# Optimization experiments

Hardware: AMD Instinct MI355X
Metric: run time of the kernel (lower is better)

The kernel has to match this reference:

```python
import jax, jax.numpy as jnp
import numpy as np

N = 50000      # nodes
E = 800000     # edges (avg degree 16)
H = 128        # hidden_nf
NORM_FACTOR = 100.0   # normalization_factor, aggregation 'sum'
NORM_CONST = 1.0      # norm_constant (effective_constant = max(1, 1.0))
EPS = 1e-8


def silu(v):
    return v * jax.nn.sigmoid(v)


def setup_inputs() -> dict:
    key = jax.random.key(0)
    ks = jax.random.split(key, 16)
    IN_E = 2 * H + 2  # edge MLP input: h[row] | h[col] | [radial, edge_attr]

    def w(k, shape, scale=0.05):
        return jax.random.normal(k, shape, dtype=jnp.float32) * scale

    return {
        "h": jax.random.normal(ks[0], (N, H), dtype=jnp.float32),
        "x": jax.random.normal(ks[1], (N, 3), dtype=jnp.float32),
        "edge_index": jax.random.randint(ks[2], (2, E), 0, N, dtype=jnp.int32),
        "edge_attr": jax.random.normal(ks[3], (E, 1), dtype=jnp.float32),
        "node_mask": jnp.ones((N, 1), dtype=jnp.float32),
        "edge_mask": jnp.ones((E, 1), dtype=jnp.float32),
        # 2 stacked GCL layers (identical shapes -> stacked on leading dim)
        "gcl_e_w1": w(ks[4], (2, IN_E, H)), "gcl_e_b1": jnp.zeros((2, H), jnp.float32),
        "gcl_e_w2": w(ks[5], (2, H, H)),    "gcl_e_b2": jnp.zeros((2, H), jnp.float32),
        "gcl_a_w":  w(ks[6], (2, H, 1)),    "gcl_a_b":  jnp.zeros((2, 1), jnp.float32),
        "gcl_n_w1": w(ks[7], (2, 2 * H, H)),"gcl_n_b1": jnp.zeros((2, H), jnp.float32),
        "gcl_n_w2": w(ks[8], (2, H, H)),    "gcl_n_b2": jnp.zeros((2, H), jnp.float32),
        # EquivariantUpdate coord MLP (last layer xavier gain 0.001 -> tiny, no bias)
        "c_w1": w(ks[9], (IN_E, H)), "c_b1": jnp.zeros((H,), jnp.float32),
        "c_w2": w(ks[10], (H, H)),   "c_b2": jnp.zeros((H,), jnp.float32),
        "c_w3": w(ks[11], (H, 1), 0.001),
    }


def reference(h, x, edge_index, edge_attr, node_mask, edge_mask,
              gcl_e_w1, gcl_e_b1, gcl_e_w2, gcl_e_b2, gcl_a_w, gcl_a_b,
              gcl_n_w1, gcl_n_b1, gcl_n_w2, gcl_n_b2,
              c_w1, c_b1, c_w2, c_b2, c_w3):
    row, col = edge_index[0], edge_index[1]
    n_nodes = h.shape[0]

    # coord2diff
    diff = x[row] - x[col]                                  # [E,3]
    radial = jnp.sum(diff * diff, axis=1, keepdims=True)    # [E,1]
    norm = jnp.sqrt(radial + EPS)
    coord_diff = diff / (norm + NORM_CONST)

    # edge_attr = cat([distances, edge_attr])  -> edge_feat_nf = 2
    ea = jnp.concatenate([radial, edge_attr], axis=1)       # [E,2]

    # n_layers=2 GCLs with attention
    for i in range(2):
        einp = jnp.concatenate([h[row], h[col], ea], axis=1)             # [E,258]
        mij = silu(silu(einp @ gcl_e_w1[i] + gcl_e_b1[i]) @ gcl_e_w2[i] + gcl_e_b2[i])
        att = jax.nn.sigmoid(mij @ gcl_a_w[i] + gcl_a_b[i])
        ef = mij * att * edge_mask                                       # [E,H]
        agg = jax.ops.segment_sum(ef, row, num_segments=n_nodes) / NORM_FACTOR
        ninp = jnp.concatenate([h, agg], axis=1)                         # [N,2H]
        h = h + (silu(ninp @ gcl_n_w1[i] + gcl_n_b1[i]) @ gcl_n_w2[i] + gcl_n_b2[i])
        h = h * node_mask

    # EquivariantUpdate (tanh=False, reflection_equiv=True -> no cross term)
    einp = jnp.concatenate([h[row], h[col], ea], axis=1)
    phi = silu(silu(einp @ c_w1 + c_b1) @ c_w2 + c_b2) @ c_w3            # [E,1]
    trans = coord_diff * phi * edge_mask                                 # [E,3]
    aggx = jax.ops.segment_sum(trans, row, num_segments=n_nodes) / NORM_FACTOR
    x = (x + aggx) * node_mask

    h = h * node_mask
    return (h, x)
```

## Files before the change

kernel.cpp:

```cpp
#include <hip/hip_runtime.h>
#include <hip/hip_bf16.h>
#include <math.h>
#include <string.h>

#define DEV __device__ __forceinline__

typedef __bf16 bf16;
typedef bf16 bf16x8 __attribute__((ext_vector_type(8)));
typedef bf16 bf16x2 __attribute__((ext_vector_type(2)));
typedef float f32x4 __attribute__((ext_vector_type(4)));
typedef unsigned int uint;

constexpr int N_NODES = 50000;
constexpr int N_EDGES = 800000;
constexpr int H = 128;
constexpr int NB_SCAN = (N_NODES + 255) / 256;

DEV float fsilu(float x) { return x / (1.f + __expf(-x)); }
DEV float fsigmoid(float x) { return 1.f / (1.f + __expf(-x)); }


__global__ void transpose_pad_kernel(bf16* __restrict__ dst, const float* __restrict__ src,
                                     int K, int Nf, int KP) {
    int idx = blockIdx.x * 256 + threadIdx.x;
    if (idx >= Nf * KP) return;
    int n = idx / KP, k = idx - n * KP;
    dst[idx] = (k < K) ? (bf16)src[k * Nf + n] : (bf16)0.f;
}

__global__ void h_init_kernel(const float* __restrict__ h, float* __restrict__ h_cur,
                              bf16* __restrict__ h_bf, int n) {
    int i = blockIdx.x * 256 + threadIdx.x;
    if (i < n) { float v = h[i]; h_cur[i] = v; h_bf[i] = (bf16)v; }
}

__global__ void ea_kernel(const float* __restrict__ x, const int* __restrict__ ei,
                          const float* __restrict__ eattr, bf16* __restrict__ ea_bf) {
    int e = blockIdx.x * 256 + threadIdx.x;
    if (e >= N_EDGES) return;
    int r = ei[e], c = ei[N_EDGES + e];
    float dx = x[r * 3 + 0] - x[c * 3 + 0];
    float dy = x[r * 3 + 1] - x[c * 3 + 1];
    float dz = x[r * 3 + 2] - x[c * 3 + 2];
    float radial = dx * dx + dy * dy + dz * dz;
    ea_bf[e * 2 + 0] = (bf16)radial;
    ea_bf[e * 2 + 1] = (bf16)eattr[e];
}

__global__ void out_h_kernel(const float* __restrict__ h_cur, const float* __restrict__ nmask,
                             float* __restrict__ out) {
    int i = blockIdx.x * 256 + threadIdx.x;
    if (i < N_NODES * H) out[i] = h_cur[i] * nmask[i >> 7];
}


__global__ void count_kernel(const int* __restrict__ ei, int* __restrict__ deg) {
    int e = blockIdx.x * 256 + threadIdx.x;
    if (e < N_EDGES) atomicAdd(&deg[ei[e]], 1);
}

__global__ void scan1_kernel(const int* __restrict__ deg, int* __restrict__ off,
                             int* __restrict__ bsum) {
    __shared__ int s[256];
    int t = threadIdx.x, i = blockIdx.x * 256 + t;
    int v = (i < N_NODES) ? deg[i] : 0;
    s[t] = v;
    __syncthreads();
#pragma unroll
    for (int st = 1; st < 256; st <<= 1) {
        int x = (t >= st) ? s[t - st] : 0;
        __syncthreads();
        s[t] += x;
        __syncthreads();
    }
    if (i < N_NODES) off[i] = s[t] - v;
    if (t == 255) bsum[blockIdx.x] = s[255];
}

__global__ void scan2_kernel(int* __restrict__ bsum) {
    __shared__ int s[256];
    int t = threadIdx.x;
    int v = (t < NB_SCAN) ? bsum[t] : 0;
    s[t] = v;
    __syncthreads();
#pragma unroll
    for (int st = 1; st < 256; st <<= 1) {
        int x = (t >= st) ? s[t - st] : 0;
        __syncthreads();
        s[t] += x;
        __syncthreads();
    }
    if (t < NB_SCAN) bsum[t] = s[t] - v;
}

__global__ void scan3_kernel(int* __restrict__ off, int* __restrict__ cursor,
                             const int* __restrict__ bsum) {
    int i = blockIdx.x * 256 + threadIdx.x;
    if (i >= N_NODES) return;
    int o = off[i] + bsum[blockIdx.x];
    off[i] = o;
    cursor[i] = o;
}

__global__ void fill_kernel(const int* __restrict__ ei, int* __restrict__ cursor,
                            int* __restrict__ eids) {
    int e = blockIdx.x * 256 + threadIdx.x;
    if (e >= N_EDGES) return;
    int slot = atomicAdd(&cursor[ei[e]], 1);
    eids[slot] = e;
}


__global__ __launch_bounds__(256) void gather_h_kernel(
    const bf16* __restrict__ ef, const int* __restrict__ off, const int* __restrict__ deg,
    const int* __restrict__ eids, bf16* __restrict__ agg_bf) {
    int t = threadIdx.x, lane = t & 63, wv = t >> 6;
    int n = blockIdx.x * 4 + wv;
    if (n >= N_NODES) return;
    int st = off[n], dg = deg[n];
    float s0 = 0.f, s1 = 0.f;
    for (int k = 0; k < dg; ++k) {
        int e = eids[st + k];
        uint v = *(const uint*)(ef + (size_t)e * H + lane * 2);
        s0 += __uint_as_float(v << 16);
        s1 += __uint_as_float(v & 0xffff0000u);
    }
    bf16x2 o;
    o[0] = (bf16)(s0 * 0.01f);
    o[1] = (bf16)(s1 * 0.01f);
    *(bf16x2*)(agg_bf + (size_t)n * H + lane * 2) = o;
}

__global__ __launch_bounds__(256) void gather_x_kernel(
    const float* __restrict__ trans, const int* __restrict__ off, const int* __restrict__ deg,
    const int* __restrict__ eids, const float* __restrict__ x, const float* __restrict__ nmask,
    float* __restrict__ outx) {
    int t = threadIdx.x, lane = t & 63, wv = t >> 6;
    int n = blockIdx.x * 4 + wv;
    if (n >= N_NODES) return;
    int st = off[n], dg = deg[n];
    float sx = 0.f, sy = 0.f, sz = 0.f;
    for (int k = lane; k < dg; k += 64) {
        int e = eids[st + k];
        sx += trans[e * 3 + 0];
        sy += trans[e * 3 + 1];
        sz += trans[e * 3 + 2];
    }
#pragma unroll
    for (int m = 1; m < 64; m <<= 1) {
        sx += __shfl_xor(sx, m);
        sy += __shfl_xor(sy, m);
        sz += __shfl_xor(sz, m);
    }
    if (lane == 0) {
        float nm = nmask[n];
        outx[n * 3 + 0] = (x[n * 3 + 0] + sx * 0.01f) * nm;
        outx[n * 3 + 1] = (x[n * 3 + 1] + sy * 0.01f) * nm;
        outx[n * 3 + 2] = (x[n * 3 + 2] + sz * 0.01f) * nm;
    }
}


template <int KCHUNKS, int ASTRIDE, int BSTRIDE>
DEV void wave_gemm(const bf16* A_lds, const bf16* __restrict__ Bt,
                   f32x4 (&acc)[4][2], int lr, int lg, int wv) {
#pragma unroll
    for (int kk = 0; kk < KCHUNKS; ++kk) {
        int ko = kk * 32 + lg * 8;
        bf16x8 a[4], b[2];
#pragma unroll
        for (int er = 0; er < 4; ++er)
            a[er] = *(const bf16x8*)(A_lds + (er * 16 + lr) * ASTRIDE + ko);
#pragma unroll
        for (int j = 0; j < 2; ++j)
            b[j] = *(const bf16x8*)(Bt + (size_t)((wv * 2 + j) * 16 + lr) * BSTRIDE + ko);
#pragma unroll
        for (int er = 0; er < 4; ++er)
#pragma unroll
            for (int j = 0; j < 2; ++j)
                acc[er][j] = __builtin_amdgcn_mfma_f32_16x16x32_bf16(a[er], b[j], acc[er][j], 0, 0, 0);
    }
}

DEV void epi_silu_store(const f32x4 (&acc)[4][2], const float* __restrict__ bias,
                        bf16* out_lds, int OSTRIDE, int lr, int lg, int wv) {
    float b0 = bias[(wv * 2 + 0) * 16 + lr];
    float b1 = bias[(wv * 2 + 1) * 16 + lr];
#pragma unroll
    for (int er = 0; er < 4; ++er) {
#pragma unroll
        for (int j = 0; j < 2; ++j) {
            float bb = j ? b1 : b0;
            int fcol = (wv * 2 + j) * 16 + lr;
#pragma unroll
            for (int r = 0; r < 4; ++r) {
                int rrow = er * 16 + lg * 4 + r;
                out_lds[rrow * OSTRIDE + fcol] = (bf16)fsilu(acc[er][j][r] + bb);
            }
        }
    }
}

DEV void epi_silu_store_swz(const f32x4 (&acc)[4][2], const float* __restrict__ bias,
                            bf16* out_lds, int lr, int lg, int wv) {
    float b0 = bias[(wv * 2 + 0) * 16 + lr];
    float b1 = bias[(wv * 2 + 1) * 16 + lr];
#pragma unroll
    for (int er = 0; er < 4; ++er) {
#pragma unroll
        for (int j = 0; j < 2; ++j) {
            float bb = j ? b1 : b0;
            int fcol = (wv * 2 + j) * 16 + lr;
#pragma unroll
            for (int r = 0; r < 4; ++r) {
                int rrow = er * 16 + lg * 4 + r;
                int sl = (fcol >> 3) ^ (rrow & 7);
                out_lds[rrow * 128 + sl * 8 + (fcol & 7)] = (bf16)fsilu(acc[er][j][r] + bb);
            }
        }
    }
}

template <int MODE>
__global__ __launch_bounds__(256, 4) void edge_kernel(
    const bf16* __restrict__ h_bf, const bf16* __restrict__ ea_bf,
    const int* __restrict__ ei, const float* __restrict__ emask,
    const bf16* __restrict__ w1t, const float* __restrict__ b1,
    const bf16* __restrict__ w2t, const float* __restrict__ b2,
    const float* __restrict__ avec, const float* __restrict__ abias,
    const float* __restrict__ xg, bf16* __restrict__ efout, float* __restrict__ trans) {
    __shared__ __align__(16) bf16 AR[64 * 128];
    __shared__ __align__(16) bf16 AC[64 * 128];
    __shared__ __align__(16) float avec_l[128];
    __shared__ int row_l[64];
    __shared__ int col_l[64];
    __shared__ float em_l[64];

    int t = threadIdx.x, lane = t & 63, wv = t >> 6;
    int lr = lane & 15, lg = lane >> 4;
    int ebase = blockIdx.x * 64;

    {
        int rsub = lane >> 4;
        int slot = lane & 15;
#pragma unroll
        for (int u = 0; u < 4; ++u) {
            int r = wv * 16 + u * 4 + rsub;
            int nr = ei[ebase + r];
            int sl = slot ^ (r & 7);
            const bf16* gp = h_bf + (size_t)nr * H + sl * 8;
            __builtin_amdgcn_global_load_lds(
                (const __attribute__((address_space(1))) void*)gp,
                (__attribute__((address_space(3))) void*)&AR[(wv * 16 + u * 4) * 128],
                16, 0, 0);
        }
#pragma unroll
        for (int u = 0; u < 4; ++u) {
            int r = wv * 16 + u * 4 + rsub;
            int nc = ei[N_EDGES + ebase + r];
            int sl = slot ^ (r & 7);
            const bf16* gp = h_bf + (size_t)nc * H + sl * 8;
            __builtin_amdgcn_global_load_lds(
                (const __attribute__((address_space(1))) void*)gp,
                (__attribute__((address_space(3))) void*)&AC[(wv * 16 + u * 4) * 128],
                16, 0, 0);
        }
    }
    if (t < 64) {
        int e = ebase + t;
        row_l[t] = ei[e];
        col_l[t] = ei[N_EDGES + e];
        em_l[t] = emask[e];
    } else if (t < 192) {
        avec_l[t - 64] = avec[t - 64];
    }

    uint eau[4];
#pragma unroll
    for (int er = 0; er < 4; ++er)
        eau[er] = *(const uint*)(ea_bf + (size_t)(ebase + er * 16 + lr) * 2);

    const bf16* bp0 = w1t + (size_t)((wv * 2 + 0) * 16 + lr) * 288 + lg * 8;
    const bf16* bp1 = w1t + (size_t)((wv * 2 + 1) * 16 + lr) * 288 + lg * 8;

    __syncthreads();

    f32x4 acc[4][2];
#pragma unroll
    for (int er = 0; er < 4; ++er)
#pragma unroll
        for (int j = 0; j < 2; ++j) acc[er][j] = (f32x4)0.f;

#pragma unroll
    for (int kk = 0; kk < 8; ++kk) {
        const bf16* Ab = (kk < 4) ? AR : AC;
        int k4 = kk & 3;
        bf16x8 a[4], b[2];
        b[0] = *(const bf16x8*)(bp0 + kk * 32);
        b[1] = *(const bf16x8*)(bp1 + kk * 32);
#pragma unroll
        for (int er = 0; er < 4; ++er) {
            int sl = (k4 * 4 + lg) ^ (lr & 7);
            a[er] = *(const bf16x8*)(Ab + (er * 16 + lr) * 128 + sl * 8);
        }
#pragma unroll
        for (int er = 0; er < 4; ++er)
#pragma unroll
            for (int j = 0; j < 2; ++j)
                acc[er][j] = __builtin_amdgcn_mfma_f32_16x16x32_bf16(a[er], b[j], acc[er][j], 0, 0, 0);
    }
    {
        bf16x8 a[4], b[2];
        b[0] = *(const bf16x8*)(bp0 + 8 * 32);
        b[1] = *(const bf16x8*)(bp1 + 8 * 32);
#pragma unroll
        for (int er = 0; er < 4; ++er) {
            bf16x8 f = (bf16x8)(bf16)0.f;
            if (lg == 0) {
                bf16x2 ep;
                memcpy(&ep, &eau[er], 4);
                f[0] = ep[0];
                f[1] = ep[1];
            }
            a[er] = f;
        }
#pragma unroll
        for (int er = 0; er < 4; ++er)
#pragma unroll
            for (int j = 0; j < 2; ++j)
                acc[er][j] = __builtin_amdgcn_mfma_f32_16x16x32_bf16(a[er], b[j], acc[er][j], 0, 0, 0);
    }
    __syncthreads();

    epi_silu_store_swz(acc, b1, AR, lr, lg, wv);
    __syncthreads();

    f32x4 acc2[4][2];
#pragma unroll
    for (int er = 0; er < 4; ++er)
#pragma unroll
        for (int j = 0; j < 2; ++j) acc2[er][j] = (f32x4)0.f;
    {
        const bf16* cp0 = w2t + (size_t)((wv * 2 + 0) * 16 + lr) * 128 + lg * 8;
        const bf16* cp1 = w2t + (size_t)((wv * 2 + 1) * 16 + lr) * 128 + lg * 8;
#pragma unroll
        for (int kk = 0; kk < 4; ++kk) {
            bf16x8 a[4], b[2];
            b[0] = *(const bf16x8*)(cp0 + kk * 32);
            b[1] = *(const bf16x8*)(cp1 + kk * 32);
#pragma unroll
            for (int er = 0; er < 4; ++er) {
                int sl = (kk * 4 + lg) ^ (lr & 7);
                a[er] = *(const bf16x8*)(AR + (er * 16 + lr) * 128 + sl * 8);
            }
#pragma unroll
            for (int er = 0; er < 4; ++er)
#pragma unroll
                for (int j = 0; j < 2; ++j)
                    acc2[er][j] = __builtin_amdgcn_mfma_f32_16x16x32_bf16(a[er], b[j], acc2[er][j], 0, 0, 0);
        }
    }

    bf16* mij = AC;
    epi_silu_store_swz(acc2, b2, mij, lr, lg, wv);
    __syncthreads();

    int el = t >> 2, q = t & 3;
    float part = 0.f;
    bf16x8 mv[4];
#pragma unroll
    for (int c = 0; c < 4; ++c) {
        int sl = (q * 4 + c) ^ (el & 7);
        mv[c] = *(const bf16x8*)(mij + el * 128 + sl * 8);
        f32x4 av0 = *(const f32x4*)(avec_l + q * 32 + c * 8);
        f32x4 av1 = *(const f32x4*)(avec_l + q * 32 + c * 8 + 4);
#pragma unroll
        for (int jj = 0; jj < 4; ++jj) part += (float)mv[c][jj] * av0[jj];
#pragma unroll
        for (int jj = 0; jj < 4; ++jj) part += (float)mv[c][4 + jj] * av1[jj];
    }
    part += __shfl_xor(part, 1);
    part += __shfl_xor(part, 2);

    if (MODE == 0) {
        float att = fsigmoid(part + abias[0]);
        float scale = att * em_l[el];
        bf16* edst = efout + (size_t)(ebase + el) * H + q * 32;
#pragma unroll
        for (int c = 0; c < 4; ++c) {
            bf16x8 o;
#pragma unroll
            for (int jj = 0; jj < 8; ++jj) o[jj] = (bf16)((float)mv[c][jj] * scale);
            *(bf16x8*)(edst + c * 8) = o;
        }
    } else {
        if (q == 0) {
            int rr = row_l[el], cc = col_l[el];
            float dx = xg[rr * 3 + 0] - xg[cc * 3 + 0];
            float dy = xg[rr * 3 + 1] - xg[cc * 3 + 1];
            float dz = xg[rr * 3 + 2] - xg[cc * 3 + 2];
            float radial = dx * dx + dy * dy + dz * dz;
            float inv = 1.f / (sqrtf(radial + 1e-8f) + 1.f);
            float s = part * em_l[el] * inv;
            int e = ebase + el;
            trans[e * 3 + 0] = dx * s;
            trans[e * 3 + 1] = dy * s;
            trans[e * 3 + 2] = dz * s;
        }
    }
}

__global__ __launch_bounds__(256, 2) void node_kernel(
    float* __restrict__ h_cur, bf16* __restrict__ h_bf, const bf16* __restrict__ agg_bf,
    const bf16* __restrict__ w1t, const float* __restrict__ b1,
    const bf16* __restrict__ w2t, const float* __restrict__ b2,
    const float* __restrict__ nmask) {
    constexpr int SRN = 264;
    constexpr int TRN = 136;
    __shared__ __align__(16) bf16 ninp[64 * SRN];
    __shared__ __align__(16) bf16 t1[64 * TRN];

    int t = threadIdx.x, lane = t & 63, wv = t >> 6;
    int lr = lane & 15, lg = lane >> 4;
    int nbase = blockIdx.x * 64;

    {
        int nl = t >> 2, q = t & 3;
        int node = nbase + nl;
        bf16* dst = ninp + nl * SRN;
        if (node < N_NODES) {
            const float4* hr = (const float4*)(h_cur + (size_t)node * H);
            const bf16* ar = agg_bf + (size_t)node * H;
#pragma unroll
            for (int pp = 0; pp < 8; ++pp) {
                int ch = pp * 4 + q;
                float4 v = hr[ch];
                dst[ch * 4 + 0] = (bf16)v.x; dst[ch * 4 + 1] = (bf16)v.y;
                dst[ch * 4 + 2] = (bf16)v.z; dst[ch * 4 + 3] = (bf16)v.w;
            }
#pragma unroll
            for (int pp = 0; pp < 4; ++pp) {
                int ch = pp * 4 + q;
                *(bf16x8*)(dst + 128 + ch * 8) = *(const bf16x8*)(ar + ch * 8);
            }
        } else {
#pragma unroll
            for (int pp = 0; pp < 8; ++pp) {
                int ch = pp * 4 + q;
#pragma unroll
                for (int k = 0; k < 4; ++k) {
                    dst[ch * 4 + k] = (bf16)0.f;
                    dst[128 + ch * 4 + k] = (bf16)0.f;
                }
            }
        }
    }
    __syncthreads();

    f32x4 acc[4][2];
#pragma unroll
    for (int er = 0; er < 4; ++er)
#pragma unroll
        for (int j = 0; j < 2; ++j) acc[er][j] = (f32x4)0.f;
    wave_gemm<8, SRN, 256>(ninp, w1t, acc, lr, lg, wv);
    epi_silu_store(acc, b1, t1, TRN, lr, lg, wv);
    __syncthreads();

    f32x4 acc2[4][2];
#pragma unroll
    for (int er = 0; er < 4; ++er)
#pragma unroll
        for (int j = 0; j < 2; ++j) acc2[er][j] = (f32x4)0.f;
    wave_gemm<4, TRN, 128>(t1, w2t, acc2, lr, lg, wv);

    float bb0 = b2[(wv * 2 + 0) * 16 + lr];
    float bb1 = b2[(wv * 2 + 1) * 16 + lr];
#pragma unroll
    for (int er = 0; er < 4; ++er) {
#pragma unroll
        for (int j = 0; j < 2; ++j) {
            float bb = j ? bb1 : bb0;
            int feat = (wv * 2 + j) * 16 + lr;
#pragma unroll
            for (int r = 0; r < 4; ++r) {
                int node = nbase + er * 16 + lg * 4 + r;
                if (node < N_NODES) {
                    size_t idx = (size_t)node * H + feat;
                    float nm = nmask[node];
                    float v = (h_cur[idx] + acc2[er][j][r] + bb) * nm;
                    h_cur[idx] = v;
                    h_bf[idx] = (bf16)v;
                }
            }
        }
    }
}

extern "C" void kernel_launch(void* const* d_in, const int* in_sizes, int n_in,
                              void* d_out, int out_size, void* d_ws, size_t ws_size,
                              hipStream_t stream) {
    (void)in_sizes; (void)n_in; (void)out_size; (void)ws_size;
    const float* h_in  = (const float*)d_in[0];
    const float* x_in  = (const float*)d_in[1];
    const int*   ei    = (const int*)d_in[2];
    const float* eattr = (const float*)d_in[3];
    const float* nmask = (const float*)d_in[4];
    const float* emask = (const float*)d_in[5];
    const float* e_w1  = (const float*)d_in[6];
    const float* e_b1  = (const float*)d_in[7];
    const float* e_w2  = (const float*)d_in[8];
    const float* e_b2  = (const float*)d_in[9];
    const float* a_w   = (const float*)d_in[10];
    const float* a_b   = (const float*)d_in[11];
    const float* n_w1  = (const float*)d_in[12];
    const float* n_b1  = (const float*)d_in[13];
    const float* n_w2  = (const float*)d_in[14];
    const float* n_b2  = (const float*)d_in[15];
    const float* c_w1  = (const float*)d_in[16];
    const float* c_b1  = (const float*)d_in[17];
    const float* c_w2  = (const float*)d_in[18];
    const float* c_b2  = (const float*)d_in[19];
    const float* c_w3  = (const float*)d_in[20];
    float* out = (float*)d_out;

    char* p = (char*)d_ws;
    auto alloc = [&](size_t bytes) { char* r = p; p += (bytes + 255) & ~(size_t)255; return r; };
    float* h_cur  = (float*)alloc((size_t)N_NODES * H * 4);
    bf16*  h_bf   = (bf16*) alloc((size_t)N_NODES * H * 2);
    bf16*  agg_bf = (bf16*) alloc((size_t)N_NODES * H * 2);
    bf16*  ea_bf  = (bf16*) alloc((size_t)N_EDGES * 2 * 2);
    bf16*  ef     = (bf16*) alloc((size_t)N_EDGES * H * 2);
    float* trans  = (float*)ef;
    int*   deg    = (int*)  alloc((size_t)N_NODES * 4);
    int*   off    = (int*)  alloc((size_t)N_NODES * 4);
    int*   cursor = (int*)  alloc((size_t)N_NODES * 4);
    int*   bsum   = (int*)  alloc((size_t)NB_SCAN * 4);
    int*   eids   = (int*)  alloc((size_t)N_EDGES * 4);
    bf16*  e_w1t  = (bf16*) alloc((size_t)2 * 128 * 288 * 2);
    bf16*  e_w2t  = (bf16*) alloc((size_t)2 * 128 * 128 * 2);
    bf16*  n_w1t  = (bf16*) alloc((size_t)2 * 128 * 256 * 2);
    bf16*  n_w2t  = (bf16*) alloc((size_t)2 * 128 * 128 * 2);
    bf16*  c_w1t  = (bf16*) alloc((size_t)128 * 288 * 2);
    bf16*  c_w2t  = (bf16*) alloc((size_t)128 * 128 * 2);

    auto tp = [&](bf16* dst, const float* src, int K, int KP) {
        int tot = 128 * KP;
        transpose_pad_kernel<<<(tot + 255) / 256, 256, 0, stream>>>(dst, src, K, 128, KP);
    };
    tp(e_w1t, e_w1, 258, 288);               tp(e_w1t + 128 * 288, e_w1 + 258 * 128, 258, 288);
    tp(e_w2t, e_w2, 128, 128);               tp(e_w2t + 128 * 128, e_w2 + 128 * 128, 128, 128);
    tp(n_w1t, n_w1, 256, 256);               tp(n_w1t + 128 * 256, n_w1 + 256 * 128, 256, 256);
    tp(n_w2t, n_w2, 128, 128);               tp(n_w2t + 128 * 128, n_w2 + 128 * 128, 128, 128);
    tp(c_w1t, c_w1, 258, 288);
    tp(c_w2t, c_w2, 128, 128);

    h_init_kernel<<<(N_NODES * H + 255) / 256, 256, 0, stream>>>(h_in, h_cur, h_bf, N_NODES * H);
    ea_kernel<<<(N_EDGES + 255) / 256, 256, 0, stream>>>(x_in, ei, eattr, ea_bf);

    hipMemsetAsync(deg, 0, (size_t)N_NODES * 4, stream);
    count_kernel<<<(N_EDGES + 255) / 256, 256, 0, stream>>>(ei, deg);
    scan1_kernel<<<NB_SCAN, 256, 0, stream>>>(deg, off, bsum);
    scan2_kernel<<<1, 256, 0, stream>>>(bsum);
    scan3_kernel<<<NB_SCAN, 256, 0, stream>>>(off, cursor, bsum);
    fill_kernel<<<(N_EDGES + 255) / 256, 256, 0, stream>>>(ei, cursor, eids);

    int ngrid = (N_NODES + 3) / 4;
    for (int i = 0; i < 2; ++i) {
        edge_kernel<0><<<N_EDGES / 64, 256, 0, stream>>>(
            h_bf, ea_bf, ei, emask,
            e_w1t + (size_t)i * 128 * 288, e_b1 + i * H,
            e_w2t + (size_t)i * 128 * 128, e_b2 + i * H,
            a_w + i * H, a_b + i, nullptr, ef, nullptr);
        gather_h_kernel<<<ngrid, 256, 0, stream>>>(ef, off, deg, eids, agg_bf);
        node_kernel<<<(N_NODES + 63) / 64, 256, 0, stream>>>(
            h_cur, h_bf, agg_bf,
            n_w1t + (size_t)i * 128 * 256, n_b1 + i * H,
            n_w2t + (size_t)i * 128 * 128, n_b2 + i * H, nmask);
    }
    edge_kernel<1><<<N_EDGES / 64, 256, 0, stream>>>(
        h_bf, ea_bf, ei, emask,
        c_w1t, c_b1, c_w2t, c_b2, c_w3, nullptr, x_in, nullptr, trans);
    gather_x_kernel<<<ngrid, 256, 0, stream>>>(trans, off, deg, eids, x_in, nmask,
                                               out + (size_t)N_NODES * H);

    out_h_kernel<<<(N_NODES * H + 255) / 256, 256, 0, stream>>>(h_cur, nmask, out);
}
```

Measured before the change: 977.4 us.

## Process edges in row-sorted order so gathers read contiguous edge outputs

Edge kernels now walk edges in CSR (row-sorted) order through eids, writing edge features and coordinate translations to sorted slots. The gather kernels can then stream contiguous rows instead of doing an indirect eids lookup per edge. Consecutive edges in a block share the same row node, which may improve cache reuse of h[row]. The edge kernel gains an extra indirection, and the first five weight chunks are preloaded into registers before the barrier, which raises register pressure.

```diff
diff --git a/kernel.cpp b/kernel.cpp
--- a/kernel.cpp
+++ b/kernel.cpp
@@ -113,15 +113,15 @@
 
 __global__ __launch_bounds__(256) void gather_h_kernel(
     const bf16* __restrict__ ef, const int* __restrict__ off, const int* __restrict__ deg,
-    const int* __restrict__ eids, bf16* __restrict__ agg_bf) {
+    bf16* __restrict__ agg_bf) {
     int t = threadIdx.x, lane = t & 63, wv = t >> 6;
     int n = blockIdx.x * 4 + wv;
     if (n >= N_NODES) return;
     int st = off[n], dg = deg[n];
+    const bf16* bp = ef + (size_t)st * H + lane * 2;
     float s0 = 0.f, s1 = 0.f;
     for (int k = 0; k < dg; ++k) {
-        int e = eids[st + k];
-        uint v = *(const uint*)(ef + (size_t)e * H + lane * 2);
+        uint v = *(const uint*)(bp + (size_t)k * H);
         s0 += __uint_as_float(v << 16);
         s1 += __uint_as_float(v & 0xffff0000u);
     }
@@ -133,18 +133,17 @@
 
 __global__ __launch_bounds__(256) void gather_x_kernel(
     const float* __restrict__ trans, const int* __restrict__ off, const int* __restrict__ deg,
-    const int* __restrict__ eids, const float* __restrict__ x, const float* __restrict__ nmask,
-    float* __restrict__ outx) {
+    const float* __restrict__ x, const float* __restrict__ nmask, float* __restrict__ outx) {
     int t = threadIdx.x, lane = t & 63, wv = t >> 6;
     int n = blockIdx.x * 4 + wv;
     if (n >= N_NODES) return;
     int st = off[n], dg = deg[n];
     float sx = 0.f, sy = 0.f, sz = 0.f;
     for (int k = lane; k < dg; k += 64) {
-        int e = eids[st + k];
-        sx += trans[e * 3 + 0];
-        sy += trans[e * 3 + 1];
-        sz += trans[e * 3 + 2];
+        const float* tp = trans + (size_t)(st + k) * 3;
+        sx += tp[0];
+        sy += tp[1];
+        sz += tp[2];
     }
 #pragma unroll
     for (int m = 1; m < 64; m <<= 1) {
@@ -225,6 +224,7 @@
 __global__ __launch_bounds__(256, 4) void edge_kernel(
     const bf16* __restrict__ h_bf, const bf16* __restrict__ ea_bf,
     const int* __restrict__ ei, const float* __restrict__ emask,
+    const int* __restrict__ eids,
     const bf16* __restrict__ w1t, const float* __restrict__ b1,
     const bf16* __restrict__ w2t, const float* __restrict__ b2,
     const float* __restrict__ avec, const float* __restrict__ abias,
@@ -246,28 +246,24 @@
 #pragma unroll
         for (int u = 0; u < 4; ++u) {
             int r = wv * 16 + u * 4 + rsub;
-            int nr = ei[ebase + r];
+            int e = eids[ebase + r];
+            int nr = ei[e];
+            int nc = ei[N_EDGES + e];
             int sl = slot ^ (r & 7);
-            const bf16* gp = h_bf + (size_t)nr * H + sl * 8;
+            const bf16* gpr = h_bf + (size_t)nr * H + sl * 8;
             __builtin_amdgcn_global_load_lds(
-                (const __attribute__((address_space(1))) void*)gp,
+                (const __attribute__((address_space(1))) void*)gpr,
                 (__attribute__((address_space(3))) void*)&AR[(wv * 16 + u * 4) * 128],
                 16, 0, 0);
-        }
-#pragma unroll
-        for (int u = 0; u < 4; ++u) {
-            int r = wv * 16 + u * 4 + rsub;
-            int nc = ei[N_EDGES + ebase + r];
-            int sl = slot ^ (r & 7);
-            const bf16* gp = h_bf + (size_t)nc * H + sl * 8;
+            const bf16* gpc = h_bf + (size_t)nc * H + sl * 8;
             __builtin_amdgcn_global_load_lds(
-                (const __attribute__((address_space(1))) void*)gp,
+                (const __attribute__((address_space(1))) void*)gpc,
                 (__attribute__((address_space(3))) void*)&AC[(wv * 16 + u * 4) * 128],
                 16, 0, 0);
         }
     }
     if (t < 64) {
-        int e = ebase + t;
+        int e = eids[ebase + t];
         row_l[t] = ei[e];
         col_l[t] = ei[N_EDGES + e];
         em_l[t] = emask[e];
@@ -277,11 +273,20 @@
 
     uint eau[4];
 #pragma unroll
-    for (int er = 0; er < 4; ++er)
-        eau[er] = *(const uint*)(ea_bf + (size_t)(ebase + er * 16 + lr) * 2);
+    for (int er = 0; er < 4; ++er) {
+        int e = eids[ebase + er * 16 + lr];
+        eau[er] = *(const uint*)(ea_bf + (size_t)e * 2);
+    }
 
     const bf16* bp0 = w1t + (size_t)((wv * 2 + 0) * 16 + lr) * 288 + lg * 8;
     const bf16* bp1 = w1t + (size_t)((wv * 2 + 1) * 16 + lr) * 288 + lg * 8;
+
+    bf16x8 bv0[5], bv1[5];
+#pragma unroll
+    for (int kk = 0; kk < 5; ++kk) {
+        bv0[kk] = *(const bf16x8*)(bp0 + kk * 32);
+        bv1[kk] = *(const bf16x8*)(bp1 + kk * 32);
+    }
 
     __syncthreads();
 
@@ -296,8 +301,8 @@
         const bf16* Ab = (kk < 4) ? AR : AC;
         int k4 = kk & 3;
         bf16x8 a[4], b[2];
-        b[0] = *(const bf16x8*)(bp0 + kk * 32);
-        b[1] = *(const bf16x8*)(bp1 + kk * 32);
+        b[0] = (kk < 5) ? bv0[kk] : *(const bf16x8*)(bp0 + kk * 32);
+        b[1] = (kk < 5) ? bv1[kk] : *(const bf16x8*)(bp1 + kk * 32);
 #pragma unroll
         for (int er = 0; er < 4; ++er) {
             int sl = (k4 * 4 + lg) ^ (lr & 7);
@@ -402,10 +407,10 @@
             float radial = dx * dx + dy * dy + dz * dz;
             float inv = 1.f / (sqrtf(radial + 1e-8f) + 1.f);
             float s = part * em_l[el] * inv;
-            int e = ebase + el;
-            trans[e * 3 + 0] = dx * s;
-            trans[e * 3 + 1] = dy * s;
-            trans[e * 3 + 2] = dz * s;
+            int sI = ebase + el;
+            trans[sI * 3 + 0] = dx * s;
+            trans[sI * 3 + 1] = dy * s;
+            trans[sI * 3 + 2] = dz * s;
         }
     }
 }
@@ -567,20 +572,20 @@
     int ngrid = (N_NODES + 3) / 4;
     for (int i = 0; i < 2; ++i) {
         edge_kernel<0><<<N_EDGES / 64, 256, 0, stream>>>(
-            h_bf, ea_bf, ei, emask,
+            h_bf, ea_bf, ei, emask, eids,
             e_w1t + (size_t)i * 128 * 288, e_b1 + i * H,
             e_w2t + (size_t)i * 128 * 128, e_b2 + i * H,
             a_w + i * H, a_b + i, nullptr, ef, nullptr);
-        gather_h_kernel<<<ngrid, 256, 0, stream>>>(ef, off, deg, eids, agg_bf);
+        gather_h_kernel<<<ngrid, 256, 0, stream>>>(ef, off, deg, agg_bf);
         node_kernel<<<(N_NODES + 63) / 64, 256, 0, stream>>>(
             h_cur, h_bf, agg_bf,
             n_w1t + (size_t)i * 128 * 256, n_b1 + i * H,
             n_w2t + (size_t)i * 128 * 128, n_b2 + i * H, nmask);
     }
     edge_kernel<1><<<N_EDGES / 64, 256, 0, stream>>>(
-        h_bf, ea_bf, ei, emask,
+        h_bf, ea_bf, ei, emask, eids,
         c_w1t, c_b1, c_w2t, c_b2, c_w3, nullptr, x_in, nullptr, trans);
-    gather_x_kernel<<<ngrid, 256, 0, stream>>>(trans, off, deg, eids, x_in, nmask,
+    gather_x_kernel<<<ngrid, 256, 0, stream>>>(trans, off, deg, x_in, nmask,
                                                out + (size_t)N_NODES * H);
 
     out_h_kernel<<<(N_NODES * H + 255) / 256, 256, 0, stream>>>(h_cur, nmask, out);
```

Measured after the change: 957.3 us. 1.02x faster.
